# Kernel optimization log

Measured on AMD Instinct MI355X. Metric: run time of the kernel, lower is better.

The kernel has to match this reference:

```python
import jax, jax.numpy as jnp
import numpy as np

B, IMG, P, NP, S = 16, 224, 16, 196, 197
D, H, DH, L, FF = 768, 12, 64, 12, 3072


def setup_inputs() -> dict:
    key = jax.random.key(0)
    ks = jax.random.split(key, 16)
    nrm = lambda k, shape: jax.random.normal(k, shape, jnp.float32) * 0.02
    return {
        "x": jax.random.normal(ks[0], (B, IMG, IMG, 3), jnp.float32),
        "cls": jnp.zeros((1, 1, D), jnp.float32),
        "pos_emb": nrm(ks[1], (S, D)),
        "Wp": nrm(ks[2], (P * P * 3, D)), "bp": jnp.zeros((D,), jnp.float32),
        "Wq": nrm(ks[3], (L, D, D)), "bq": jnp.zeros((L, D), jnp.float32),
        "Wk": nrm(ks[4], (L, D, D)), "bk": jnp.zeros((L, D), jnp.float32),
        "Wv": nrm(ks[5], (L, D, D)), "bv": jnp.zeros((L, D), jnp.float32),
        "Wo": nrm(ks[6], (L, D, D)), "bo": jnp.zeros((L, D), jnp.float32),
        "ln1g": jnp.ones((L, D), jnp.float32), "ln1b": jnp.zeros((L, D), jnp.float32),
        "ln2g": jnp.ones((L, D), jnp.float32), "ln2b": jnp.zeros((L, D), jnp.float32),
        "W1": nrm(ks[7], (L, D, FF)), "b1": jnp.zeros((L, FF), jnp.float32),
        "W2": nrm(ks[8], (L, FF, D)), "b2": jnp.zeros((L, D), jnp.float32),
        "lnfg": jnp.ones((D,), jnp.float32), "lnfb": jnp.zeros((D,), jnp.float32),
    }


def _ln(y, g, b, eps):
    m = y.mean(-1, keepdims=True)
    v = ((y - m) ** 2).mean(-1, keepdims=True)
    return (y - m) / jnp.sqrt(v + eps) * g + b


def _gelu(z):
    # tanh-approx GeLU, exactly as in the source module
    return 0.5 * z * (1.0 + jnp.tanh(np.sqrt(2.0 / np.pi) * (z + 0.044715 * z ** 3)))


def reference(x, cls, pos_emb, Wp, bp, Wq, bq, Wk, bk, Wv, bv, Wo, bo,
              ln1g, ln1b, ln2g, ln2b, W1, b1, W2, b2, lnfg, lnfb):
    Bb = x.shape[0]
    g = IMG // P  # 14 patches per side
    # tf.image.extract_patches with VALID, stride==size: row-major patch flatten
    patches = x.reshape(Bb, g, P, g, P, 3).transpose(0, 1, 3, 2, 4, 5).reshape(Bb, NP, P * P * 3)
    h = patches @ Wp + bp                               # [B, 196, D]
    h = jnp.concatenate([jnp.broadcast_to(cls, (Bb, 1, D)), h], axis=1) + pos_emb  # [B, S, D]

    scale = np.float32(1.0 / np.sqrt(DH))

    def block(h, p):
        wq, bq_, wk, bk_, wv, bv_, wo, bo_, g1, gb1, g2, gb2, w1, b1_, w2, b2_ = p
        y = _ln(h, g1, gb1, 1e-6)
        q = (y @ wq + bq_).reshape(Bb, S, H, DH).transpose(0, 2, 1, 3)  # [B,H,S,dh]
        k = (y @ wk + bk_).reshape(Bb, S, H, DH).transpose(0, 2, 1, 3)
        v = (y @ wv + bv_).reshape(Bb, S, H, DH).transpose(0, 2, 1, 3)
        w = jax.nn.softmax(jnp.einsum('bhqd,bhkd->bhqk', q, k) * scale, axis=-1)
        att = jnp.einsum('bhqk,bhkd->bhqd', w, v)       # [B,H,S,dh]
        # NOTE: in the source the two Permutes cancel, so the "concat" is a raw
        # reshape of the [B,H,S,dh] tensor to [B,S,D] (heads interleaved). Faithful.
        concat = att.reshape(Bb, S, D)
        h1 = h + concat @ wo + bo_
        y = _ln(h1, g2, gb2, 1e-6)
        y = _gelu(y @ w1 + b1_) @ w2 + b2_
        return h1 + y, None

    h, _ = jax.lax.scan(block, h, (Wq, bq, Wk, bk, Wv, bv, Wo, bo,
                                   ln1g, ln1b, ln2g, ln2b, W1, b1, W2, b2))
    return _ln(h, lnfg, lnfb, 1e-3)  # final Keras LayerNorm, default eps=1e-3
```

## Files before the change

kernel.cpp:

```cpp
#include <hip/hip_runtime.h>
#include <cstdint>
#include <cstddef>

#define DD   768
#define HHN  12
#define SS   197
#define FFD  3072
#define MROWS 3152
#define MPAD  3200
#define PROWS 3136

typedef __attribute__((ext_vector_type(4))) float  f32x4;
typedef __attribute__((ext_vector_type(8))) __bf16 bf16x8;
typedef __attribute__((ext_vector_type(4))) __bf16 bf16x4;

__global__ __launch_bounds__(256) void w2b_k(const float* __restrict__ W, __bf16* __restrict__ Wb, int N)
{
  __shared__ float Ws[64][65];
  const int t = threadIdx.x;
  const int n0 = blockIdx.x * 64, k0 = blockIdx.y * 64;
  const int nl = t & 63, kq = t >> 6;
  #pragma unroll
  for (int i = 0; i < 16; ++i) {
    const int k = kq * 16 + i;
    Ws[k][nl] = W[(size_t)(k0 + k) * N + n0 + nl];
  }
  __syncthreads();
  #pragma unroll
  for (int r = 0; r < 2; ++r) {
    const int c = r * 256 + t;
    const int kh = c >> 6, n = c & 63;
    bf16x8 v;
    #pragma unroll
    for (int j = 0; j < 8; ++j) v[j] = (__bf16)Ws[kh * 8 + j][n];
    *(bf16x8*)(Wb + ((size_t)((k0 >> 3) + kh) * N + n0 + n) * 8) = v;
  }
}

template<int BN, int NMAT, int MODE, bool GELU_, bool STOREBF, bool VT>
__global__ __launch_bounds__(256) void gemm_k(
    const __bf16* __restrict__ A,
    const __bf16* __restrict__ Bb0, const __bf16* __restrict__ Bb1, const __bf16* __restrict__ Bb2,
    const float* __restrict__ bias0, const float* __restrict__ bias1, const float* __restrict__ bias2,
    float* __restrict__ Cf, __bf16* __restrict__ Cb, __bf16* __restrict__ vt,
    int N, int Kloc, int Kstride)
{
  const int mt = blockIdx.x & 31;
  if (mt >= 25) return;
  const int m0 = mt * 128;
  const int n0 = (blockIdx.x >> 5) * BN;
  const int kz = blockIdx.y;
  const size_t kOff = (size_t)kz * Kloc;

  constexpr int BUFB = (BN == 128) ? 16384 : 12288;
  __shared__ char lds[3 * BUFB];
  const int tid = threadIdx.x;

  int mat = 0, nB = n0, NBw = N;
  const __bf16* Bbp = Bb0; const float* biasp = bias0;
  if (NMAT == 3) {
    mat = n0 / DD; nB = n0 - mat * DD; NBw = DD;
    Bbp   = (mat == 0) ? Bb0   : ((mat == 1) ? Bb1   : Bb2);
    biasp = (mat == 0) ? bias0 : ((mat == 1) ? bias1 : bias2);
  }

  constexpr int NC = (BN == 128) ? 4 : 2;
  f32x4 acc[4][NC];
  const f32x4 z4 = {0.f, 0.f, 0.f, 0.f};
  #pragma unroll
  for (int i = 0; i < 4; ++i)
    #pragma unroll
    for (int j = 0; j < NC; ++j) acc[i][j] = z4;

  const int lane = tid & 63;
  const int wv = tid >> 6;
  const int wr = wv >> 1, wc = wv & 1;
  const int arow = tid & 127, akh = tid >> 7;

  const int nKB = Kloc >> 5;

  auto issue = [&](int kt, int buf) {
    const int k0 = kt << 5;
    char* Ab = lds + buf * BUFB;
    char* Bbl = Ab + 8192;
    {
      const __bf16* ga0 = A + (size_t)(m0 + arow) * Kstride + kOff + k0 + akh * 8;
      auto g0 = (__attribute__((address_space(1))) unsigned int*)(uintptr_t)ga0;
      auto g1 = (__attribute__((address_space(1))) unsigned int*)(uintptr_t)(ga0 + 16);
      auto l0 = (__attribute__((address_space(3))) unsigned int*)(uintptr_t)(Ab + wv * 1024);
      auto l1 = (__attribute__((address_space(3))) unsigned int*)(uintptr_t)(Ab + 4096 + wv * 1024);
      __builtin_amdgcn_global_load_lds(g0, l0, 16, 0, 0);
      __builtin_amdgcn_global_load_lds(g1, l1, 16, 0, 0);
    }
    if (BN == 128) {
      #pragma unroll
      for (int r = 0; r < 2; ++r) {
        const int c = r * 256 + tid;
        const int g = c >> 7, col = c & 127;
        const __bf16* gb = Bbp + ((size_t)(((kOff + k0) >> 3) + g) * NBw + nB + col) * 8;
        auto gp = (__attribute__((address_space(1))) unsigned int*)(uintptr_t)gb;
        auto lp = (__attribute__((address_space(3))) unsigned int*)(uintptr_t)(Bbl + r * 4096 + wv * 1024);
        __builtin_amdgcn_global_load_lds(gp, lp, 16, 0, 0);
      }
    } else {
      const __bf16* gb = Bbp + ((size_t)(((kOff + k0) >> 3) + wv) * NBw + nB + lane) * 8;
      auto gp = (__attribute__((address_space(1))) unsigned int*)(uintptr_t)gb;
      auto lp = (__attribute__((address_space(3))) unsigned int*)(uintptr_t)(Bbl + wv * 1024);
      __builtin_amdgcn_global_load_lds(gp, lp, 16, 0, 0);
    }
  };

  constexpr int WAITIMM = (BN == 128) ? 0xF78  : 0xF76 ;

  issue(0, 0);
  issue(nKB > 1 ? 1 : 0, 1);

  int cb = 0, wb = 2;
  const int q = lane >> 4, r16 = lane & 15;
  for (int kb = 0; kb < nKB; ++kb) {
    __builtin_amdgcn_sched_barrier(0);
    __builtin_amdgcn_s_barrier();
    const int nxt = kb + 2;
    issue(nxt < nKB ? nxt : nKB - 1, wb);
    __builtin_amdgcn_s_waitcnt(WAITIMM);
    __builtin_amdgcn_s_barrier();
    __builtin_amdgcn_sched_barrier(0);

    const char* Ab = lds + cb * BUFB;
    const char* Bbl = Ab + 8192;
    const char* pa = Ab + q * 2048 + (wr * 64 + r16) * 16;
    const char* pb = (BN == 128) ? (Bbl + q * 2048 + (wc * 64 + r16) * 16)
                                 : (Bbl + q * 1024 + (wc * 32 + r16) * 16);
    bf16x8 af[4], bfv[NC];
    #pragma unroll
    for (int i = 0; i < 4; ++i) af[i]  = *(const bf16x8*)(pa + i * 256);
    #pragma unroll
    for (int i = 0; i < NC; ++i) bfv[i] = *(const bf16x8*)(pb + i * 256);
    #pragma unroll
    for (int ri = 0; ri < 4; ++ri)
      #pragma unroll
      for (int ci = 0; ci < NC; ++ci)
        acc[ri][ci] = __builtin_amdgcn_mfma_f32_16x16x32_bf16(af[ri], bfv[ci], acc[ri][ci], 0, 0, 0);

    cb = (cb == 2) ? 0 : cb + 1;
    wb = (wb == 2) ? 0 : wb + 1;
  }
  __builtin_amdgcn_s_waitcnt(0);

  const int q4 = (lane >> 4) * 4, c16 = lane & 15;
  #pragma unroll
  for (int ci = 0; ci < NC; ++ci) {
    const int n = n0 + ((BN == 128) ? wc * 64 : wc * 32) + ci * 16 + c16;
    const float bsv = (MODE == 1 && kz != 0) ? 0.f
                      : biasp[(NMAT == 3) ? (n - mat * DD) : n];
    #pragma unroll
    for (int ri = 0; ri < 4; ++ri) {
      const int mb = m0 + wr * 64 + ri * 16 + q4;
      #pragma unroll
      for (int rg = 0; rg < 4; ++rg) {
        float v = acc[ri][ci][rg] + bsv;
        const int row = mb + rg;
        if (VT && NMAT == 3 && mat == 2) {
          const int b = row / SS;
          if (b < 16) {
            const int s = row - b * SS;
            const int nloc = n - 2 * DD;
            const int hh = nloc >> 6, d = nloc & 63;
            vt[((size_t)(b * HHN + hh) * 28 + (s >> 3)) * 512 + d * 8 + (s & 7)] = (__bf16)v;
          }
        } else {
          const size_t off = (size_t)row * N + n;
          if (MODE == 1) {
            atomicAdd(&Cf[off], v);
          } else {
            if (GELU_) {
              const float zz = v;
              const float a = 0.7978845608028654f * (zz + 0.044715f * zz * zz * zz);
              v = 0.5f * zz * (2.0f - 2.0f / (1.0f + __expf(2.0f * a)));
            }
            if (STOREBF) Cb[off] = (__bf16)v; else Cf[off] = v;
          }
        }
      }
    }
  }
}

__global__ __launch_bounds__(256) void attn_k(const __bf16* __restrict__ qkv,
                                              const __bf16* __restrict__ vt,
                                              __bf16* __restrict__ att)
{
  __shared__ char als[58240];
  const int t = threadIdx.x;
  const int qt = blockIdx.x, bh = blockIdx.y;
  const int b = bh / HHN, hh = bh % HHN;
  const int r0 = qt * 64;

  bf16x8 vstage[7];
  #pragma unroll
  for (int i = 0; i < 7; ++i)
    vstage[i] = *(const bf16x8*)(vt + (size_t)bh * 14336 + (size_t)(t + i * 256) * 8);

  #pragma unroll
  for (int i = 0; i < 7; ++i) {
    const int c = t + i * 256;
    const int kh = c & 7, s = c >> 3;
    const int sg = s < SS ? s : (SS - 1);
    const bf16x8 v = *(const bf16x8*)(qkv + (size_t)(b * SS + sg) * 2304 + DD + hh * 64 + kh * 8);
    *(bf16x8*)(als + kh * 3600 + s * 16) = v;
  }
  #pragma unroll
  for (int i = 0; i < 2; ++i) {
    const int c = t + i * 256;
    const int qr = c & 63, dh8 = c >> 6;
    const int rr = r0 + qr;
    const int sg = rr < SS ? rr : (SS - 1);
    const bf16x8 v = *(const bf16x8*)(qkv + (size_t)(b * SS + sg) * 2304 + hh * 64 + dh8 * 8);
    *(bf16x8*)(als + 28800 + dh8 * 1040 + qr * 16) = v;
  }
  __syncthreads();

  const int w = t >> 6, lane = t & 63;
  const int q = lane >> 4, c16 = lane & 15;
  const f32x4 z4 = {0.f, 0.f, 0.f, 0.f};

  f32x4 acc[13];
  #pragma unroll
  for (int nt = 0; nt < 13; ++nt) acc[nt] = z4;
  #pragma unroll
  for (int kk = 0; kk < 2; ++kk) {
    const bf16x8 af = *(const bf16x8*)(als + 28800 + (kk * 4 + q) * 1040 + (w * 16 + c16) * 16);
    #pragma unroll
    for (int nt = 0; nt < 13; ++nt) {
      const bf16x8 bf_ = *(const bf16x8*)(als + (kk * 4 + q) * 3600 + (nt * 16 + c16) * 16);
      acc[nt] = __builtin_amdgcn_mfma_f32_16x16x32_bf16(af, bf_, acc[nt], 0, 0, 0);
    }
  }
  __syncthreads();

  float inv[4];
  #pragma unroll
  for (int rg = 0; rg < 4; ++rg) {
    float mx = -1e30f;
    #pragma unroll
    for (int nt = 0; nt < 13; ++nt) {
      const bool val = (nt < 12) || (c16 < 5);
      const float sv = acc[nt][rg] * 0.125f;
      if (val) mx = fmaxf(mx, sv);
    }
    #pragma unroll
    for (int m = 1; m < 16; m <<= 1) mx = fmaxf(mx, __shfl_xor(mx, m, 16));
    float sm = 0.f;
    #pragma unroll
    for (int nt = 0; nt < 13; ++nt) {
      const bool val = (nt < 12) || (c16 < 5);
      const float e = val ? __expf(acc[nt][rg] * 0.125f - mx) : 0.f;
      acc[nt][rg] = e; sm += e;
    }
    #pragma unroll
    for (int m = 1; m < 16; m <<= 1) sm += __shfl_xor(sm, m, 16);
    inv[rg] = 1.f / sm;
  }

  #pragma unroll
  for (int nt = 0; nt < 14; ++nt) {
    #pragma unroll
    for (int rg = 0; rg < 4; ++rg) {
      const int s = nt * 16 + c16;
      const int qr = w * 16 + q * 4 + rg;
      const float pv = (nt < 13) ? acc[nt][rg] * inv[rg] : 0.f;
      *(__bf16*)(als + (s >> 3) * 1040 + qr * 16 + (s & 7) * 2) = (__bf16)pv;
    }
  }
  #pragma unroll
  for (int i = 0; i < 7; ++i) {
    const int c = t + i * 256;
    *(bf16x8*)(als + 29120 + (c >> 6) * 1040 + (c & 63) * 16) = vstage[i];
  }
  __syncthreads();

  f32x4 o[4];
  #pragma unroll
  for (int dt = 0; dt < 4; ++dt) o[dt] = z4;
  #pragma unroll
  for (int kk = 0; kk < 7; ++kk) {
    const bf16x8 af = *(const bf16x8*)(als + (kk * 4 + q) * 1040 + (w * 16 + c16) * 16);
    #pragma unroll
    for (int dt = 0; dt < 4; ++dt) {
      const bf16x8 bf_ = *(const bf16x8*)(als + 29120 + (kk * 4 + q) * 1040 + (dt * 16 + c16) * 16);
      o[dt] = __builtin_amdgcn_mfma_f32_16x16x32_bf16(af, bf_, o[dt], 0, 0, 0);
    }
  }
  #pragma unroll
  for (int dt = 0; dt < 4; ++dt) {
    #pragma unroll
    for (int rg = 0; rg < 4; ++rg) {
      const int r = r0 + w * 16 + q * 4 + rg;
      if (r < SS)
        att[((size_t)bh * SS + r) * 64 + dt * 16 + c16] = (__bf16)o[dt][rg];
    }
  }
}

template<bool OUTBF>
__global__ __launch_bounds__(256) void ln_k(const float* __restrict__ X,
    const float* __restrict__ g, const float* __restrict__ be, float eps,
    __bf16* __restrict__ Yb, float* __restrict__ Yf)
{
  const int row = blockIdx.x * 4 + (threadIdx.x >> 6), l = threadIdx.x & 63;
  const f32x4* xr = (const f32x4*)(X + (size_t)row * DD);
  f32x4 v[3];
  #pragma unroll
  for (int j = 0; j < 3; ++j) v[j] = xr[l + j * 64];
  float s = 0.f;
  #pragma unroll
  for (int j = 0; j < 3; ++j) s += v[j][0] + v[j][1] + v[j][2] + v[j][3];
  #pragma unroll
  for (int m = 1; m < 64; m <<= 1) s += __shfl_xor(s, m, 64);
  const float mean = s * (1.f / 768.f);
  float vs = 0.f;
  #pragma unroll
  for (int j = 0; j < 3; ++j)
    #pragma unroll
    for (int e = 0; e < 4; ++e) { const float d = v[j][e] - mean; vs += d * d; }
  #pragma unroll
  for (int m = 1; m < 64; m <<= 1) vs += __shfl_xor(vs, m, 64);
  const float rstd = rsqrtf(vs * (1.f / 768.f) + eps);
  const f32x4* gp = (const f32x4*)g; const f32x4* bp = (const f32x4*)be;
  #pragma unroll
  for (int j = 0; j < 3; ++j) {
    const int c4 = l + j * 64;
    const f32x4 gg = gp[c4], bb = bp[c4];
    if (OUTBF) {
      bf16x4 o;
      #pragma unroll
      for (int e = 0; e < 4; ++e) o[e] = (__bf16)((v[j][e] - mean) * rstd * gg[e] + bb[e]);
      *(bf16x4*)(Yb + (size_t)row * DD + c4 * 4) = o;
    } else {
      f32x4 o;
      #pragma unroll
      for (int e = 0; e < 4; ++e) o[e] = (v[j][e] - mean) * rstd * gg[e] + bb[e];
      *(f32x4*)(Yf + (size_t)row * DD + c4 * 4) = o;
    }
  }
}

__global__ __launch_bounds__(256) void im2col_k(const float* __restrict__ x, __bf16* __restrict__ patches)
{
  const int idx = blockIdx.x * 256 + threadIdx.x;
  const int row = idx / 768, col = idx % 768;
  float v = 0.f;
  if (row < PROWS) {
    const int b = row / 196, p = row % 196;
    const int py = p / 14, px = p % 14;
    const int r = col / 48, rem = col % 48, c = rem / 3, ch = rem % 3;
    v = x[((size_t)(b * 224 + py * 16 + r) * 224 + (px * 16 + c)) * 3 + ch];
  }
  patches[idx] = (__bf16)v;
}

__global__ __launch_bounds__(256) void assemble_k(const float* __restrict__ tmp, const float* __restrict__ cls,
    const float* __restrict__ pos, float* __restrict__ h)
{
  const int idx = blockIdx.x * 256 + threadIdx.x;
  const int row = idx / 192, qc = (idx % 192) * 4;
  f32x4 v = {0.f, 0.f, 0.f, 0.f};
  if (row < MROWS) {
    const int b = row / SS, s2 = row % SS;
    if (s2 == 0) v = *(const f32x4*)(cls + qc);
    else         v = *(const f32x4*)(tmp + (size_t)(b * 196 + s2 - 1) * 768 + qc);
    const f32x4 p = *(const f32x4*)(pos + (size_t)s2 * 768 + qc);
    v += p;
  }
  *(f32x4*)(h + (size_t)row * 768 + qc) = v;
}

extern "C" void kernel_launch(void* const* d_in, const int* in_sizes, int n_in,
                              void* d_out, int out_size, void* d_ws, size_t ws_size,
                              hipStream_t stream)
{
  (void)in_sizes; (void)n_in; (void)out_size;
  const float* x    = (const float*)d_in[0];
  const float* cls  = (const float*)d_in[1];
  const float* pos  = (const float*)d_in[2];
  const float* Wp   = (const float*)d_in[3];
  const float* bp   = (const float*)d_in[4];
  const float* Wq   = (const float*)d_in[5];
  const float* bq   = (const float*)d_in[6];
  const float* Wk   = (const float*)d_in[7];
  const float* bk   = (const float*)d_in[8];
  const float* Wv   = (const float*)d_in[9];
  const float* bv   = (const float*)d_in[10];
  const float* Wo   = (const float*)d_in[11];
  const float* bo   = (const float*)d_in[12];
  const float* ln1g = (const float*)d_in[13];
  const float* ln1b = (const float*)d_in[14];
  const float* ln2g = (const float*)d_in[15];
  const float* ln2b = (const float*)d_in[16];
  const float* W1   = (const float*)d_in[17];
  const float* b1   = (const float*)d_in[18];
  const float* W2   = (const float*)d_in[19];
  const float* b2   = (const float*)d_in[20];
  const float* lnfg = (const float*)d_in[21];
  const float* lnfb = (const float*)d_in[22];

  char* ws = (char*)d_ws;
  float*  h    = (float*) (ws + 0);
  __bf16* y    = (__bf16*)(ws + 9830400);
  __bf16* qkv  = (__bf16*)(ws + 14745600);
  float*  tmp  = (float*) (ws + 14745600);
  __bf16* att  = (__bf16*)(ws + 29491200);
  __bf16* mffn = (__bf16*)(ws + 34406400);
  __bf16* patches = (__bf16*)(ws + 34406400);
  __bf16* Wpb = (__bf16*)(ws + 54067200);
  __bf16* Wqb = (__bf16*)(ws + 55246848);
  __bf16* Wkb = (__bf16*)(ws + 69402624);
  __bf16* Wvb = (__bf16*)(ws + 83558400);
  __bf16* Wob = (__bf16*)(ws + 97714176);
  __bf16* W1b = (__bf16*)(ws + 111869952);
  __bf16* W2b = (__bf16*)(ws + 168493056);
  __bf16* vt  = (__bf16*)(ws + 225116160);
  if (ws_size < 230621184) return;

  w2b_k<<<dim3(12, 12),  256, 0, stream>>>(Wp, Wpb, DD);
  w2b_k<<<dim3(12, 144), 256, 0, stream>>>(Wq, Wqb, DD);
  w2b_k<<<dim3(12, 144), 256, 0, stream>>>(Wk, Wkb, DD);
  w2b_k<<<dim3(12, 144), 256, 0, stream>>>(Wv, Wvb, DD);
  w2b_k<<<dim3(12, 144), 256, 0, stream>>>(Wo, Wob, DD);
  w2b_k<<<dim3(48, 144), 256, 0, stream>>>(W1, W1b, FFD);
  w2b_k<<<dim3(12, 576), 256, 0, stream>>>(W2, W2b, DD);

  im2col_k<<<MPAD * 768 / 256, 256, 0, stream>>>(x, patches);
  gemm_k<64,1,0,false,false,false><<<12*32, 256, 0, stream>>>(
      patches, Wpb,Wpb,Wpb, bp,bp,bp, tmp, nullptr, nullptr, DD, DD, DD);
  assemble_k<<<MPAD * 192 / 256, 256, 0, stream>>>(tmp, cls, pos, h);

  for (int l = 0; l < 12; ++l) {
    const size_t wDD = (size_t)l * DD * DD, wFF = (size_t)l * DD * FFD;
    ln_k<true><<<MROWS / 4, 256, 0, stream>>>(h, ln1g + l*DD, ln1b + l*DD, 1e-6f, y, nullptr);
    gemm_k<128,3,0,false,true,true><<<18*32, 256, 0, stream>>>(
        y, Wqb + wDD, Wkb + wDD, Wvb + wDD,
        bq + l*DD, bk + l*DD, bv + l*DD, nullptr, qkv, vt, 3*DD, DD, DD);
    attn_k<<<dim3(4, 192), 256, 0, stream>>>(qkv, vt, att);
    gemm_k<64,1,1,false,false,false><<<12*32, 256, 0, stream>>>(
        att, Wob + wDD, nullptr, nullptr, bo + l*DD, nullptr, nullptr,
        h, nullptr, nullptr, DD, DD, DD);
    ln_k<true><<<MROWS / 4, 256, 0, stream>>>(h, ln2g + l*DD, ln2b + l*DD, 1e-6f, y, nullptr);
    gemm_k<128,1,0,true,true,false><<<24*32, 256, 0, stream>>>(
        y, W1b + wFF, nullptr, nullptr, b1 + l*FFD, nullptr, nullptr,
        nullptr, mffn, nullptr, FFD, DD, DD);
    gemm_k<128,1,1,false,false,false><<<dim3(6*32, 2), 256, 0, stream>>>(
        mffn, W2b + wFF, nullptr, nullptr, b2 + l*DD, nullptr, nullptr,
        h, nullptr, nullptr, DD, FFD/2, FFD);
  }
  ln_k<false><<<MROWS / 4, 256, 0, stream>>>(h, lnfg, lnfb, 1e-3f, nullptr, (float*)d_out);
}
```

Before: 2.428 ms.

## Use 256x256-tile triple-buffered GEMMs with split-K partials reduced inside LayerNorm

Adds a new GEMM kernel with 512 threads, 256x256 output tiles and a three-stage global_load_lds pipeline, and uses it for the QKV, output-projection, FFN1 and FFN2 matmuls. The Wo and W2 GEMMs now write split-K partials to a scratch buffer instead of doing atomicAdd into h. A new lnsum kernel adds those partials into the residual, writes h back and applies the next LayerNorm in the same pass. The intent is more data reuse per tile and fewer atomics and separate passes over h. The cost is extra scratch memory traffic for the partials, and low tile counts (for example 48 or 96 blocks) may underfill the GPU.

```diff
diff --git a/kernel.cpp b/kernel.cpp
--- a/kernel.cpp
+++ b/kernel.cpp
@@ -9,6 +9,7 @@
 #define MROWS 3152
 #define MPAD  3200
 #define PROWS 3136
+#define PSTRIDE 2420736
 
 typedef __attribute__((ext_vector_type(4))) float  f32x4;
 typedef __attribute__((ext_vector_type(8))) __bf16 bf16x8;
@@ -186,6 +187,146 @@
   }
 }
 
+template<int NMAT, int MODE, bool GELU_, bool STOREBF, bool VT>
+__global__ __launch_bounds__(512, 2) void gemm8_k(
+    const __bf16* __restrict__ A,
+    const __bf16* __restrict__ Bb0, const __bf16* __restrict__ Bb1, const __bf16* __restrict__ Bb2,
+    const float* __restrict__ bias0, const float* __restrict__ bias1, const float* __restrict__ bias2,
+    float* __restrict__ Cf, __bf16* __restrict__ Cb, __bf16* __restrict__ vt,
+    int N, int Kloc, int Kstride)
+{
+  const int mt = blockIdx.x & 15;
+  if (mt >= 13) return;
+  const int nt = blockIdx.x >> 4;
+  const int m0 = mt * 256;
+  const int n0 = nt * 256;
+  const int kz = blockIdx.y;
+  const size_t kOff = (size_t)kz * Kloc;
+
+  __shared__ char lds[3 * 32768];
+  const int tid = threadIdx.x;
+
+  int mat = 0, nB = n0, NBw = N;
+  const __bf16* Bbp = Bb0; const float* biasp = bias0;
+  if (NMAT == 3) {
+    mat = n0 / DD; nB = n0 - mat * DD; NBw = DD;
+    Bbp   = (mat == 0) ? Bb0   : ((mat == 1) ? Bb1   : Bb2);
+    biasp = (mat == 0) ? bias0 : ((mat == 1) ? bias1 : bias2);
+  }
+
+  f32x4 acc[8][4];
+  const f32x4 z4 = {0.f, 0.f, 0.f, 0.f};
+  #pragma unroll
+  for (int i = 0; i < 8; ++i)
+    #pragma unroll
+    for (int j = 0; j < 4; ++j) acc[i][j] = z4;
+
+  const int lane = tid & 63;
+  const int wv = tid >> 6;
+  const int wr = wv >> 2, wc = wv & 3;
+  const int nKB = Kloc >> 5;
+
+  auto issue = [&](int kt, int buf) {
+    const int k0 = kt << 5;
+    char* Ab = lds + buf * 32768;
+    char* Bl = Ab + 16384;
+    #pragma unroll
+    for (int j = 0; j < 2; ++j) {
+      const int i = j * 512 + tid;
+      const int kh = i >> 8, row = i & 255;
+      int rowg = m0 + row; if (rowg > MROWS - 1) rowg = MROWS - 1;
+      const __bf16* ga = A + (size_t)rowg * Kstride + kOff + k0 + kh * 8;
+      auto gp = (__attribute__((address_space(1))) unsigned int*)(uintptr_t)ga;
+      auto lp = (__attribute__((address_space(3))) unsigned int*)(uintptr_t)(Ab + (j * 512 + wv * 64) * 16);
+      __builtin_amdgcn_global_load_lds(gp, lp, 16, 0, 0);
+    }
+    #pragma unroll
+    for (int j = 0; j < 2; ++j) {
+      const int i = j * 512 + tid;
+      const int kh = i >> 8, col = i & 255;
+      const __bf16* gb = Bbp + ((size_t)(((kOff + k0) >> 3) + kh) * NBw + nB + col) * 8;
+      auto gp = (__attribute__((address_space(1))) unsigned int*)(uintptr_t)gb;
+      auto lp = (__attribute__((address_space(3))) unsigned int*)(uintptr_t)(Bl + (j * 512 + wv * 64) * 16);
+      __builtin_amdgcn_global_load_lds(gp, lp, 16, 0, 0);
+    }
+  };
+
+  issue(0, 0);
+  issue(nKB > 1 ? 1 : 0, 1);
+
+  int cb = 0, wb = 2;
+  const int q = lane >> 4, r16 = lane & 15;
+  for (int kb = 0; kb < nKB; ++kb) {
+    __builtin_amdgcn_sched_barrier(0);
+    __builtin_amdgcn_s_barrier();
+    const int nxt = kb + 2;
+    issue(nxt < nKB ? nxt : nKB - 1, wb);
+    __builtin_amdgcn_s_waitcnt(0xF78);
+    __builtin_amdgcn_s_barrier();
+    __builtin_amdgcn_sched_barrier(0);
+
+    const char* Ab = lds + cb * 32768;
+    const char* Bl = Ab + 16384;
+    bf16x8 bfv[4];
+    #pragma unroll
+    for (int j = 0; j < 4; ++j)
+      bfv[j] = *(const bf16x8*)(Bl + q * 4096 + (wc * 64 + j * 16 + r16) * 16);
+    __builtin_amdgcn_s_setprio(1);
+    #pragma unroll
+    for (int half = 0; half < 2; ++half) {
+      bf16x8 af[4];
+      #pragma unroll
+      for (int i = 0; i < 4; ++i)
+        af[i] = *(const bf16x8*)(Ab + q * 4096 + (wr * 128 + half * 64 + i * 16 + r16) * 16);
+      #pragma unroll
+      for (int i = 0; i < 4; ++i)
+        #pragma unroll
+        for (int j = 0; j < 4; ++j)
+          acc[half * 4 + i][j] =
+            __builtin_amdgcn_mfma_f32_16x16x32_bf16(af[i], bfv[j], acc[half * 4 + i][j], 0, 0, 0);
+    }
+    __builtin_amdgcn_s_setprio(0);
+    cb = (cb == 2) ? 0 : cb + 1;
+    wb = (wb == 2) ? 0 : wb + 1;
+  }
+  __builtin_amdgcn_s_waitcnt(0);
+
+  const int q4 = (lane >> 4) * 4, c16 = lane & 15;
+  #pragma unroll
+  for (int j = 0; j < 4; ++j) {
+    const int n = n0 + wc * 64 + j * 16 + c16;
+    const float bsv = (MODE == 2 && kz != 0) ? 0.f : biasp[(NMAT == 3) ? (n - mat * DD) : n];
+    #pragma unroll
+    for (int ri = 0; ri < 8; ++ri) {
+      const int mb = m0 + wr * 128 + ri * 16 + q4;
+      #pragma unroll
+      for (int rg = 0; rg < 4; ++rg) {
+        const int row = mb + rg;
+        if (row < MROWS) {
+          float v = acc[ri][j][rg] + bsv;
+          if (VT && NMAT == 3 && mat == 2) {
+            const int b = row / SS;
+            const int s = row - b * SS;
+            const int nloc = n - 2 * DD;
+            const int hh = nloc >> 6, d = nloc & 63;
+            vt[((size_t)(b * HHN + hh) * 28 + (s >> 3)) * 512 + d * 8 + (s & 7)] = (__bf16)v;
+          } else if (MODE == 2) {
+            Cf[(size_t)kz * PSTRIDE + (size_t)row * N + n] = v;
+          } else {
+            if (GELU_) {
+              const float zz = v;
+              const float a = 0.7978845608028654f * (zz + 0.044715f * zz * zz * zz);
+              v = 0.5f * zz * (2.0f - 2.0f / (1.0f + __expf(2.0f * a)));
+            }
+            if (STOREBF) Cb[(size_t)row * N + n] = (__bf16)v;
+            else         Cf[(size_t)row * N + n] = v;
+          }
+        }
+      }
+    }
+  }
+}
+
 __global__ __launch_bounds__(256) void attn_k(const __bf16* __restrict__ qkv,
                                               const __bf16* __restrict__ vt,
                                               __bf16* __restrict__ att)
@@ -312,6 +453,60 @@
   f32x4 v[3];
   #pragma unroll
   for (int j = 0; j < 3; ++j) v[j] = xr[l + j * 64];
+  float s = 0.f;
+  #pragma unroll
+  for (int j = 0; j < 3; ++j) s += v[j][0] + v[j][1] + v[j][2] + v[j][3];
+  #pragma unroll
+  for (int m = 1; m < 64; m <<= 1) s += __shfl_xor(s, m, 64);
+  const float mean = s * (1.f / 768.f);
+  float vs = 0.f;
+  #pragma unroll
+  for (int j = 0; j < 3; ++j)
+    #pragma unroll
+    for (int e = 0; e < 4; ++e) { const float d = v[j][e] - mean; vs += d * d; }
+  #pragma unroll
+  for (int m = 1; m < 64; m <<= 1) vs += __shfl_xor(vs, m, 64);
+  const float rstd = rsqrtf(vs * (1.f / 768.f) + eps);
+  const f32x4* gp = (const f32x4*)g; const f32x4* bp = (const f32x4*)be;
+  #pragma unroll
+  for (int j = 0; j < 3; ++j) {
+    const int c4 = l + j * 64;
+    const f32x4 gg = gp[c4], bb = bp[c4];
+    if (OUTBF) {
+      bf16x4 o;
+      #pragma unroll
+      for (int e = 0; e < 4; ++e) o[e] = (__bf16)((v[j][e] - mean) * rstd * gg[e] + bb[e]);
+      *(bf16x4*)(Yb + (size_t)row * DD + c4 * 4) = o;
+    } else {
+      f32x4 o;
+      #pragma unroll
+      for (int e = 0; e < 4; ++e) o[e] = (v[j][e] - mean) * rstd * gg[e] + bb[e];
+      *(f32x4*)(Yf + (size_t)row * DD + c4 * 4) = o;
+    }
+  }
+}
+
+template<int NPART, bool OUTBF, bool WRITEH>
+__global__ __launch_bounds__(256) void lnsum_k(const float* X,
+    const float* __restrict__ P, const float* __restrict__ g, const float* __restrict__ be,
+    float eps, __bf16* __restrict__ Yb, float* __restrict__ Yf, float* Hout)
+{
+  const int row = blockIdx.x * 4 + (threadIdx.x >> 6), l = threadIdx.x & 63;
+  const f32x4* xr = (const f32x4*)(X + (size_t)row * DD);
+  f32x4 v[3];
+  #pragma unroll
+  for (int j = 0; j < 3; ++j) v[j] = xr[l + j * 64];
+  #pragma unroll
+  for (int p = 0; p < NPART; ++p) {
+    const f32x4* pr = (const f32x4*)(P + (size_t)p * PSTRIDE + (size_t)row * DD);
+    #pragma unroll
+    for (int j = 0; j < 3; ++j) v[j] += pr[l + j * 64];
+  }
+  if (WRITEH) {
+    f32x4* hw = (f32x4*)(Hout + (size_t)row * DD);
+    #pragma unroll
+    for (int j = 0; j < 3; ++j) hw[l + j * 64] = v[j];
+  }
   float s = 0.f;
   #pragma unroll
   for (int j = 0; j < 3; ++j) s += v[j][0] + v[j][1] + v[j][2] + v[j][3];
@@ -420,7 +615,8 @@
   __bf16* W1b = (__bf16*)(ws + 111869952);
   __bf16* W2b = (__bf16*)(ws + 168493056);
   __bf16* vt  = (__bf16*)(ws + 225116160);
-  if (ws_size < 230621184) return;
+  float*  pbuf = (float*)(ws + 230621184);
+  if (ws_size < 269352960) return;
 
   w2b_k<<<dim3(12, 12),  256, 0, stream>>>(Wp, Wpb, DD);
   w2b_k<<<dim3(12, 144), 256, 0, stream>>>(Wq, Wqb, DD);
@@ -435,23 +631,28 @@
       patches, Wpb,Wpb,Wpb, bp,bp,bp, tmp, nullptr, nullptr, DD, DD, DD);
   assemble_k<<<MPAD * 192 / 256, 256, 0, stream>>>(tmp, cls, pos, h);
 
+  ln_k<true><<<MROWS / 4, 256, 0, stream>>>(h, ln1g, ln1b, 1e-6f, y, nullptr);
   for (int l = 0; l < 12; ++l) {
     const size_t wDD = (size_t)l * DD * DD, wFF = (size_t)l * DD * FFD;
-    ln_k<true><<<MROWS / 4, 256, 0, stream>>>(h, ln1g + l*DD, ln1b + l*DD, 1e-6f, y, nullptr);
-    gemm_k<128,3,0,false,true,true><<<18*32, 256, 0, stream>>>(
+    gemm8_k<3,0,false,true,true><<<dim3(16*9), 512, 0, stream>>>(
         y, Wqb + wDD, Wkb + wDD, Wvb + wDD,
         bq + l*DD, bk + l*DD, bv + l*DD, nullptr, qkv, vt, 3*DD, DD, DD);
     attn_k<<<dim3(4, 192), 256, 0, stream>>>(qkv, vt, att);
-    gemm_k<64,1,1,false,false,false><<<12*32, 256, 0, stream>>>(
+    gemm8_k<1,2,false,false,false><<<dim3(16*3, 2), 512, 0, stream>>>(
         att, Wob + wDD, nullptr, nullptr, bo + l*DD, nullptr, nullptr,
-        h, nullptr, nullptr, DD, DD, DD);
-    ln_k<true><<<MROWS / 4, 256, 0, stream>>>(h, ln2g + l*DD, ln2b + l*DD, 1e-6f, y, nullptr);
-    gemm_k<128,1,0,true,true,false><<<24*32, 256, 0, stream>>>(
+        pbuf, nullptr, nullptr, DD, DD/2, DD);
+    lnsum_k<2,true,true><<<MROWS / 4, 256, 0, stream>>>(
+        h, pbuf, ln2g + l*DD, ln2b + l*DD, 1e-6f, y, nullptr, h);
+    gemm8_k<1,0,true,true,false><<<dim3(16*12), 512, 0, stream>>>(
         y, W1b + wFF, nullptr, nullptr, b1 + l*FFD, nullptr, nullptr,
         nullptr, mffn, nullptr, FFD, DD, DD);
-    gemm_k<128,1,1,false,false,false><<<dim3(6*32, 2), 256, 0, stream>>>(
+    gemm8_k<1,2,false,false,false><<<dim3(16*3, 4), 512, 0, stream>>>(
         mffn, W2b + wFF, nullptr, nullptr, b2 + l*DD, nullptr, nullptr,
-        h, nullptr, nullptr, DD, FFD/2, FFD);
-  }
-  ln_k<false><<<MROWS / 4, 256, 0, stream>>>(h, lnfg, lnfb, 1e-3f, nullptr, (float*)d_out);
-}
+        pbuf, nullptr, nullptr, DD, FFD/4, FFD);
+    if (l < 11)
+      lnsum_k<4,true,true><<<MROWS / 4, 256, 0, stream>>>(
+          h, pbuf, ln1g + (l+1)*DD, ln1b + (l+1)*DD, 1e-6f, y, nullptr, h);
+  }
+  lnsum_k<4,false,false><<<MROWS / 4, 256, 0, stream>>>(
+      h, pbuf, lnfg, lnfb, 1e-3f, nullptr, (float*)d_out, nullptr);
+}
```

New measurement: 3.194 ms. 31.5% more time.

## Replace atomic residual adds with partial buffers reduced inside fused LayerNorm

Applied to the files above, without the earlier changes.

The Wo and split-K W2 GEMMs now write plain partial results into a separate buffer instead of atomically adding into the residual stream. A new lnsum kernel adds the partials to the residual, writes the updated residual back, and computes the next LayerNorm in the same pass. The per-layer LN1 moves to the end of the previous layer. This removes fp32 atomics and one read of h per LN, at the cost of extra partial-buffer traffic and workspace.

```diff
diff --git a/kernel.cpp b/kernel.cpp
--- a/kernel.cpp
+++ b/kernel.cpp
@@ -9,6 +9,7 @@
 #define MROWS 3152
 #define MPAD  3200
 #define PROWS 3136
+#define PSTRIDE 2457600
 
 typedef __attribute__((ext_vector_type(4))) float  f32x4;
 typedef __attribute__((ext_vector_type(8))) __bf16 bf16x8;
@@ -151,7 +152,7 @@
   #pragma unroll
   for (int ci = 0; ci < NC; ++ci) {
     const int n = n0 + ((BN == 128) ? wc * 64 : wc * 32) + ci * 16 + c16;
-    const float bsv = (MODE == 1 && kz != 0) ? 0.f
+    const float bsv = ((MODE == 1 || MODE == 2) && kz != 0) ? 0.f
                       : biasp[(NMAT == 3) ? (n - mat * DD) : n];
     #pragma unroll
     for (int ri = 0; ri < 4; ++ri) {
@@ -172,6 +173,8 @@
           const size_t off = (size_t)row * N + n;
           if (MODE == 1) {
             atomicAdd(&Cf[off], v);
+          } else if (MODE == 2) {
+            Cf[(size_t)kz * PSTRIDE + off] = v;
           } else {
             if (GELU_) {
               const float zz = v;
@@ -312,6 +315,60 @@
   f32x4 v[3];
   #pragma unroll
   for (int j = 0; j < 3; ++j) v[j] = xr[l + j * 64];
+  float s = 0.f;
+  #pragma unroll
+  for (int j = 0; j < 3; ++j) s += v[j][0] + v[j][1] + v[j][2] + v[j][3];
+  #pragma unroll
+  for (int m = 1; m < 64; m <<= 1) s += __shfl_xor(s, m, 64);
+  const float mean = s * (1.f / 768.f);
+  float vs = 0.f;
+  #pragma unroll
+  for (int j = 0; j < 3; ++j)
+    #pragma unroll
+    for (int e = 0; e < 4; ++e) { const float d = v[j][e] - mean; vs += d * d; }
+  #pragma unroll
+  for (int m = 1; m < 64; m <<= 1) vs += __shfl_xor(vs, m, 64);
+  const float rstd = rsqrtf(vs * (1.f / 768.f) + eps);
+  const f32x4* gp = (const f32x4*)g; const f32x4* bp = (const f32x4*)be;
+  #pragma unroll
+  for (int j = 0; j < 3; ++j) {
+    const int c4 = l + j * 64;
+    const f32x4 gg = gp[c4], bb = bp[c4];
+    if (OUTBF) {
+      bf16x4 o;
+      #pragma unroll
+      for (int e = 0; e < 4; ++e) o[e] = (__bf16)((v[j][e] - mean) * rstd * gg[e] + bb[e]);
+      *(bf16x4*)(Yb + (size_t)row * DD + c4 * 4) = o;
+    } else {
+      f32x4 o;
+      #pragma unroll
+      for (int e = 0; e < 4; ++e) o[e] = (v[j][e] - mean) * rstd * gg[e] + bb[e];
+      *(f32x4*)(Yf + (size_t)row * DD + c4 * 4) = o;
+    }
+  }
+}
+
+template<int NPART, bool OUTBF, bool WRITEH>
+__global__ __launch_bounds__(256) void lnsum_k(const float* X,
+    const float* __restrict__ P, const float* __restrict__ g, const float* __restrict__ be,
+    float eps, __bf16* __restrict__ Yb, float* __restrict__ Yf, float* Hout)
+{
+  const int row = blockIdx.x * 4 + (threadIdx.x >> 6), l = threadIdx.x & 63;
+  const f32x4* xr = (const f32x4*)(X + (size_t)row * DD);
+  f32x4 v[3];
+  #pragma unroll
+  for (int j = 0; j < 3; ++j) v[j] = xr[l + j * 64];
+  #pragma unroll
+  for (int p = 0; p < NPART; ++p) {
+    const f32x4* pr = (const f32x4*)(P + (size_t)p * PSTRIDE + (size_t)row * DD);
+    #pragma unroll
+    for (int j = 0; j < 3; ++j) v[j] += pr[l + j * 64];
+  }
+  if (WRITEH) {
+    f32x4* hw = (f32x4*)(Hout + (size_t)row * DD);
+    #pragma unroll
+    for (int j = 0; j < 3; ++j) hw[l + j * 64] = v[j];
+  }
   float s = 0.f;
   #pragma unroll
   for (int j = 0; j < 3; ++j) s += v[j][0] + v[j][1] + v[j][2] + v[j][3];
@@ -420,7 +477,8 @@
   __bf16* W1b = (__bf16*)(ws + 111869952);
   __bf16* W2b = (__bf16*)(ws + 168493056);
   __bf16* vt  = (__bf16*)(ws + 225116160);
-  if (ws_size < 230621184) return;
+  float*  pbuf = (float*)(ws + 230621184);
+  if (ws_size < 250281984) return;
 
   w2b_k<<<dim3(12, 12),  256, 0, stream>>>(Wp, Wpb, DD);
   w2b_k<<<dim3(12, 144), 256, 0, stream>>>(Wq, Wqb, DD);
@@ -435,23 +493,28 @@
       patches, Wpb,Wpb,Wpb, bp,bp,bp, tmp, nullptr, nullptr, DD, DD, DD);
   assemble_k<<<MPAD * 192 / 256, 256, 0, stream>>>(tmp, cls, pos, h);
 
+  ln_k<true><<<MROWS / 4, 256, 0, stream>>>(h, ln1g, ln1b, 1e-6f, y, nullptr);
   for (int l = 0; l < 12; ++l) {
     const size_t wDD = (size_t)l * DD * DD, wFF = (size_t)l * DD * FFD;
-    ln_k<true><<<MROWS / 4, 256, 0, stream>>>(h, ln1g + l*DD, ln1b + l*DD, 1e-6f, y, nullptr);
     gemm_k<128,3,0,false,true,true><<<18*32, 256, 0, stream>>>(
         y, Wqb + wDD, Wkb + wDD, Wvb + wDD,
         bq + l*DD, bk + l*DD, bv + l*DD, nullptr, qkv, vt, 3*DD, DD, DD);
     attn_k<<<dim3(4, 192), 256, 0, stream>>>(qkv, vt, att);
-    gemm_k<64,1,1,false,false,false><<<12*32, 256, 0, stream>>>(
+    gemm_k<64,1,2,false,false,false><<<12*32, 256, 0, stream>>>(
         att, Wob + wDD, nullptr, nullptr, bo + l*DD, nullptr, nullptr,
-        h, nullptr, nullptr, DD, DD, DD);
-    ln_k<true><<<MROWS / 4, 256, 0, stream>>>(h, ln2g + l*DD, ln2b + l*DD, 1e-6f, y, nullptr);
+        pbuf, nullptr, nullptr, DD, DD, DD);
+    lnsum_k<1,true,true><<<MROWS / 4, 256, 0, stream>>>(
+        h, pbuf, ln2g + l*DD, ln2b + l*DD, 1e-6f, y, nullptr, h);
     gemm_k<128,1,0,true,true,false><<<24*32, 256, 0, stream>>>(
         y, W1b + wFF, nullptr, nullptr, b1 + l*FFD, nullptr, nullptr,
         nullptr, mffn, nullptr, FFD, DD, DD);
-    gemm_k<128,1,1,false,false,false><<<dim3(6*32, 2), 256, 0, stream>>>(
+    gemm_k<128,1,2,false,false,false><<<dim3(6*32, 2), 256, 0, stream>>>(
         mffn, W2b + wFF, nullptr, nullptr, b2 + l*DD, nullptr, nullptr,
-        h, nullptr, nullptr, DD, FFD/2, FFD);
-  }
-  ln_k<false><<<MROWS / 4, 256, 0, stream>>>(h, lnfg, lnfb, 1e-3f, nullptr, (float*)d_out);
-}
+        pbuf, nullptr, nullptr, DD, FFD/2, FFD);
+    if (l < 11)
+      lnsum_k<2,true,true><<<MROWS / 4, 256, 0, stream>>>(
+          h, pbuf, ln1g + (l+1)*DD, ln1b + (l+1)*DD, 1e-6f, y, nullptr, h);
+  }
+  lnsum_k<2,false,false><<<MROWS / 4, 256, 0, stream>>>(
+      h, pbuf, lnfg, lnfb, 1e-3f, nullptr, (float*)d_out, nullptr);
+}
```

After: 2.439 ms. About the same (+0.5%).
